# Kernel tuning notes

Measured on AMD Instinct MI355X. Metric: run time of the kernel, lower is better.

Reference implementation:

```python
import jax, jax.numpy as jnp
import numpy as np

B, K, H, W = 8, 32, 480, 480
N, D = 576, 1024
NUM_CLASSES, CLS_DIM, OUT = 150, 64, 256
IN_DIM = D + CLS_DIM + 5


def setup_inputs() -> dict:
    key = jax.random.key(0)
    ks = jax.random.split(key, 8)
    return {
        "feature_map": jax.random.normal(ks[0], (B, N, D), dtype=jnp.float32),
        "masks": jax.random.randint(ks[1], (B, K, H, W), 0, 2, dtype=jnp.int32),
        "class_ids": jax.random.randint(ks[2], (B, K), 0, NUM_CLASSES, dtype=jnp.int64),
        "embed_table": jax.random.normal(ks[3], (NUM_CLASSES, CLS_DIM), dtype=jnp.float32),
        "W1": jax.random.normal(ks[4], (IN_DIM, OUT), dtype=jnp.float32) * 0.02,
        "b1": jnp.zeros((OUT,), dtype=jnp.float32),
        "ln_g": jnp.ones((OUT,), dtype=jnp.float32),
        "ln_b": jnp.zeros((OUT,), dtype=jnp.float32),
        "W2": jax.random.normal(ks[5], (OUT, OUT), dtype=jnp.float32) * 0.02,
        "b2": jnp.zeros((OUT,), dtype=jnp.float32),
    }


def _geom_feats(m):
    # m: [B,K,H,W] float binary masks -> [B,K,5] (cx, cy, area_norm, bbox_w, bbox_h)
    dt = m.dtype
    area = m.sum((-2, -1))                      # [B,K]
    safe = jnp.maximum(area, 1.0)
    xs = jnp.arange(W, dtype=dt)
    ys = jnp.arange(H, dtype=dt)
    cx = jnp.einsum('bkhw,w->bk', m, xs) / safe / W
    cy = jnp.einsum('bkhw,h->bk', m, ys) / safe / H
    col = m.max(axis=2)                          # [B,K,W] column occupancy
    row = m.max(axis=3)                          # [B,K,H] row occupancy
    x_min = jnp.min(jnp.where(col > 0, xs, float(W)), axis=-1)
    x_max = jnp.max(jnp.where(col > 0, xs, -1.0), axis=-1)
    y_min = jnp.min(jnp.where(row > 0, ys, float(H)), axis=-1)
    y_max = jnp.max(jnp.where(row > 0, ys, -1.0), axis=-1)
    bbox_w = (x_max - x_min + 1.0) / W
    bbox_h = (y_max - y_min + 1.0) / H
    area_norm = area / (H * W)
    geom = jnp.stack([cx, cy, area_norm, bbox_w, bbox_h], axis=-1)  # [B,K,5]
    valid = (area >= 1.0)[..., None]
    return jnp.where(valid, geom, 0.0)


def reference(feature_map, masks, class_ids, embed_table, W1, b1, ln_g, ln_b, W2, b2):
    Hf = Wf = int(round(N ** 0.5))  # 24
    m = (masks > 0).astype(feature_map.dtype)           # [B,K,H,W]
    # nearest-neighbor downsample (PyTorch 'nearest': src = floor(dst*in/out))
    idx_h = (jnp.arange(Hf) * H) // Hf
    idx_w = (jnp.arange(Wf) * W) // Wf
    m_rs = m[:, :, idx_h][:, :, :, idx_w]               # [B,K,Hf,Wf]
    m_flat = m_rs.reshape(B, K, Hf * Wf)                # [B,K,N]
    msum = jnp.clip(m_flat.sum(-1, keepdims=True), 1e-6, None)
    pooled = jnp.einsum('bkn,bnd->bkd', m_flat, feature_map) / msum  # [B,K,D]
    geom = _geom_feats(m)                               # [B,K,5]
    cls_emb = embed_table[class_ids]                    # [B,K,CLS_DIM]
    x = jnp.concatenate([pooled, cls_emb, geom], axis=-1)  # [B,K,IN_DIM]
    h = jax.nn.gelu(x @ W1 + b1, approximate=False)
    mu = h.mean(-1, keepdims=True)
    var = jnp.mean((h - mu) ** 2, axis=-1, keepdims=True)
    hn = (h - mu) * jax.lax.rsqrt(var + 1e-5) * ln_g + ln_b
    return hn @ W2 + b2                                 # [B,K,OUT]
```

## Files before the change

### kernel.cpp

```cpp
#include <hip/hip_runtime.h>
#include <math.h>

#define Bb 8
#define Kk 32
#define Hh 480
#define Ww 480
#define Nn 576
#define Dd 1024
#define CLSD 64
#define OUTD 256
#define INDIM 1093
#define BK 256
#define PIX4 57600

__global__ __launch_bounds__(1024) void kF(const int* __restrict__ masks,
                                           const float* __restrict__ fm,
                                           const int* __restrict__ cids,
                                           const float* __restrict__ emb,
                                           const float* __restrict__ W1,
                                           const float* __restrict__ b1,
                                           const float* __restrict__ lg,
                                           const float* __restrict__ lb,
                                           const float* __restrict__ W2,
                                           const float* __restrict__ b2,
                                           float* __restrict__ out) {
  const int b    = blockIdx.x & 7;
  const int k    = blockIdx.x >> 3;
  const int bk   = b * Kk + k;
  const int t    = threadIdx.x;
  const int lane = t & 63;
  const int w    = t >> 6;

  __shared__ float  ds[576];
  __shared__ int    act[576];
  __shared__ float4 x4s[292];
  __shared__ float4 pp[4 * 256];
  __shared__ float  partial[16 * 256];
  __shared__ float  hrow[256];
  __shared__ float  red_s[16], red_q[16];
  __shared__ float  gmeta[8];
  __shared__ int s_area, s_sumx, s_sumy, s_cnt;
  __shared__ int s_minx, s_maxx, s_miny, s_maxy, nact;
  float* x = (float*)x4s;

  if (t == 0) {
    s_area = 0; s_sumx = 0; s_sumy = 0; s_cnt = 0;
    s_minx = Ww; s_maxx = -1; s_miny = Hh; s_maxy = -1;
    nact = 0;
  }
  __syncthreads();

  const int4* mp = (const int4*)(masks + (size_t)bk * (Hh * Ww));
  int area = 0, sumx = 0, sumy = 0, cntds = 0;
  int minx = Ww, maxx = -1, miny = Hh, maxy = -1;

  auto body = [&](int q, int4 v) {
    int h   = q / 120;
    int rem = q - h * 120;
    int w0  = rem * 4;
    int m0 = v.x > 0, m1 = v.y > 0, m2 = v.z > 0, m3 = v.w > 0;
    int c = m0 + m1 + m2 + m3;
    area += c;
    sumy += h * c;
    sumx += w0 * c + m1 + 2 * m2 + 3 * m3;
    if (c) {
      miny = min(miny, h);
      maxy = max(maxy, h);
      int lo = m0 ? w0 : (m1 ? w0 + 1 : (m2 ? w0 + 2 : w0 + 3));
      int hi = m3 ? w0 + 3 : (m2 ? w0 + 2 : (m1 ? w0 + 1 : w0));
      minx = min(minx, lo);
      maxx = max(maxx, hi);
    }
    int a20 = h / 20;
    int c5  = rem / 5;
    if (h == a20 * 20 && rem == c5 * 5) {
      ds[a20 * 24 + c5] = (float)m0;
      cntds += m0;
    }
  };

#pragma unroll 4
  for (int i = 0; i < 56; i++) {
    int q = t + (i << 10);
    body(q, mp[q]);
  }
  if (t < 256) {
    int q = 57344 + t;
    body(q, mp[q]);
  }

  for (int off = 32; off; off >>= 1) {
    area  += __shfl_down(area, off);
    sumx  += __shfl_down(sumx, off);
    sumy  += __shfl_down(sumy, off);
    cntds += __shfl_down(cntds, off);
    minx = min(minx, __shfl_down(minx, off));
    maxx = max(maxx, __shfl_down(maxx, off));
    miny = min(miny, __shfl_down(miny, off));
    maxy = max(maxy, __shfl_down(maxy, off));
  }
  if (lane == 0) {
    atomicAdd(&s_area, area);
    atomicAdd(&s_sumx, sumx);
    atomicAdd(&s_sumy, sumy);
    atomicAdd(&s_cnt, cntds);
    atomicMin(&s_minx, minx);
    atomicMax(&s_maxx, maxx);
    atomicMin(&s_miny, miny);
    atomicMax(&s_maxy, maxy);
  }
  __syncthreads();

  if (t == 0) {
    float areaf = (float)s_area;
    float safe  = fmaxf(areaf, 1.0f);
    float cx = ((float)s_sumx / safe) * (1.0f / Ww);
    float cy = ((float)s_sumy / safe) * (1.0f / Hh);
    float an = areaf * (1.0f / (Hh * Ww));
    float bw = (float)(s_maxx - s_minx + 1) * (1.0f / Ww);
    float bh = (float)(s_maxy - s_miny + 1) * (1.0f / Hh);
    if (s_area < 1) { cx = 0.f; cy = 0.f; an = 0.f; bw = 0.f; bh = 0.f; }
    gmeta[0] = cx; gmeta[1] = cy; gmeta[2] = an; gmeta[3] = bw; gmeta[4] = bh;
    gmeta[5] = 1.0f / fmaxf((float)s_cnt, 1e-6f);
  }
  if (t < 576 && ds[t] != 0.0f) act[atomicAdd(&nact, 1)] = t;
  if (t < 75) x[1093 + t] = 0.0f;
  __syncthreads();
  const int na = nact;

  {
    const int g   = t >> 8;
    const int col = t & 255;
    const int jb  = (na * g) >> 2;
    const int je  = (na * (g + 1)) >> 2;
    const float4* fmp = (const float4*)fm + (size_t)b * Nn * (Dd / 4);
    float ax = 0.f, ay = 0.f, az = 0.f, aw = 0.f;
    int j = jb;
    for (; j + 4 <= je; j += 4) {
      int n0 = act[j], n1 = act[j + 1], n2 = act[j + 2], n3 = act[j + 3];
      float4 f0 = fmp[n0 * (Dd / 4) + col];
      float4 f1 = fmp[n1 * (Dd / 4) + col];
      float4 f2 = fmp[n2 * (Dd / 4) + col];
      float4 f3 = fmp[n3 * (Dd / 4) + col];
      ax += f0.x + f1.x + f2.x + f3.x;
      ay += f0.y + f1.y + f2.y + f3.y;
      az += f0.z + f1.z + f2.z + f3.z;
      aw += f0.w + f1.w + f2.w + f3.w;
    }
    for (; j < je; j++) {
      float4 f = fmp[act[j] * (Dd / 4) + col];
      ax += f.x; ay += f.y; az += f.z; aw += f.w;
    }
    float4 p; p.x = ax; p.y = ay; p.z = az; p.w = aw;
    pp[g * 256 + col] = p;
  }
  __syncthreads();

  if (t < 256) {
    float inv = gmeta[5];
    float4 a0 = pp[t], a1 = pp[256 + t], a2 = pp[512 + t], a3 = pp[768 + t];
    float4 p;
    p.x = (a0.x + a1.x + a2.x + a3.x) * inv;
    p.y = (a0.y + a1.y + a2.y + a3.y) * inv;
    p.z = (a0.z + a1.z + a2.z + a3.z) * inv;
    p.w = (a0.w + a1.w + a2.w + a3.w) * inv;
    x4s[t] = p;
  } else if (t < 320) {
    x[Dd + (t - 256)] = emb[(size_t)cids[bk] * CLSD + (t - 256)];
  } else if (t < 325) {
    x[Dd + CLSD + (t - 320)] = gmeta[t - 320];
  }
  __syncthreads();

  {
    const int kbeg = w * 72;
    const int kend = min(INDIM, kbeg + 72);
    float4 acc = {0.f, 0.f, 0.f, 0.f};
    int kk = kbeg;
    for (; kk + 4 <= kend; kk += 4) {
      float4 xv = x4s[kk >> 2];
      const float* xs = (const float*)&xv;
#pragma unroll
      for (int u = 0; u < 4; u++) {
        float4 w4 = *(const float4*)(W1 + (size_t)(kk + u) * OUTD + 4 * lane);
        acc.x = fmaf(xs[u], w4.x, acc.x);
        acc.y = fmaf(xs[u], w4.y, acc.y);
        acc.z = fmaf(xs[u], w4.z, acc.z);
        acc.w = fmaf(xs[u], w4.w, acc.w);
      }
    }
    for (; kk < kend; kk++) {
      float xv = x[kk];
      float4 w4 = *(const float4*)(W1 + (size_t)kk * OUTD + 4 * lane);
      acc.x = fmaf(xv, w4.x, acc.x);
      acc.y = fmaf(xv, w4.y, acc.y);
      acc.z = fmaf(xv, w4.z, acc.z);
      acc.w = fmaf(xv, w4.w, acc.w);
    }
    *(float4*)(partial + w * 256 + 4 * lane) = acc;
  }
  __syncthreads();

  float hv = 0.f;
  if (t < 256) {
    hv = b1[t];
#pragma unroll
    for (int ww = 0; ww < 16; ww++) hv += partial[ww * 256 + t];
    hv = 0.5f * hv * (1.0f + erff(hv * 0.7071067811865475f));
  }
  {
    float s = hv, q = hv * hv;
    for (int off = 32; off; off >>= 1) {
      s += __shfl_down(s, off);
      q += __shfl_down(q, off);
    }
    if (lane == 0) { red_s[w] = s; red_q[w] = q; }
  }
  __syncthreads();
  if (t < 256) {
    float s = 0.f, q = 0.f;
#pragma unroll
    for (int ww = 0; ww < 16; ww++) { s += red_s[ww]; q += red_q[ww]; }
    float mu  = s * (1.0f / OUTD);
    float var = q * (1.0f / OUTD) - mu * mu;
    float ist = 1.0f / sqrtf(var + 1e-5f);
    hrow[t] = (hv - mu) * ist * lg[t] + lb[t];
  }
  __syncthreads();

  {
    float4 acc = {0.f, 0.f, 0.f, 0.f};
#pragma unroll
    for (int i = 0; i < 4; i++) {
      float4 h4 = ((const float4*)hrow)[w * 4 + i];
      const float* hs = (const float*)&h4;
#pragma unroll
      for (int u = 0; u < 4; u++) {
        int kk = w * 16 + i * 4 + u;
        float4 w4 = *(const float4*)(W2 + (size_t)kk * OUTD + 4 * lane);
        acc.x = fmaf(hs[u], w4.x, acc.x);
        acc.y = fmaf(hs[u], w4.y, acc.y);
        acc.z = fmaf(hs[u], w4.z, acc.z);
        acc.w = fmaf(hs[u], w4.w, acc.w);
      }
    }
    *(float4*)(partial + w * 256 + 4 * lane) = acc;
  }
  __syncthreads();

  if (t < 256) {
    float c = b2[t];
#pragma unroll
    for (int ww = 0; ww < 16; ww++) c += partial[ww * 256 + t];
    out[(size_t)bk * OUTD + t] = c;
  }
}

extern "C" void kernel_launch(void* const* d_in, const int* in_sizes, int n_in,
                              void* d_out, int out_size, void* d_ws, size_t ws_size,
                              hipStream_t stream) {
  const float* fm    = (const float*)d_in[0];
  const int*   masks = (const int*)d_in[1];
  const int*   cids  = (const int*)d_in[2];
  const float* emb   = (const float*)d_in[3];
  const float* W1    = (const float*)d_in[4];
  const float* b1    = (const float*)d_in[5];
  const float* lg    = (const float*)d_in[6];
  const float* lb    = (const float*)d_in[7];
  const float* W2    = (const float*)d_in[8];
  const float* b2    = (const float*)d_in[9];
  float* out = (float*)d_out;

  hipLaunchKernelGGL(kF, dim3(BK), dim3(1024), 0, stream, masks, fm, cids, emb,
                     W1, b1, lg, lb, W2, b2, out);
}
```

Baseline: 374.5 us.

## Warp-specialize mask stats and feature pooling/W1 GEMV to overlap

The mask sampling for the downsampled active list now happens first, with 576 direct gathers of the sampled pixels. After that the block is split: 12 warps stream the full mask for the geometry statistics, while 4 warps pool the feature rows and compute the pooled part of the W1 GEMV at the same time. The class-embedding and geometry terms of W1 are folded into the per-output epilogue, which removes several block-wide syncs and shared buffers. The risk is load imbalance: only 4 warps now carry the feature gather plus the 1024x256 W1 product, so that path may become the critical path.

```diff
diff --git a/kernel.cpp b/kernel.cpp
--- a/kernel.cpp
+++ b/kernel.cpp
@@ -31,83 +31,115 @@
   const int lane = t & 63;
   const int w    = t >> 6;
 
-  __shared__ float  ds[576];
   __shared__ int    act[576];
-  __shared__ float4 x4s[292];
-  __shared__ float4 pp[4 * 256];
+  __shared__ float4 x4s[256];
   __shared__ float  partial[16 * 256];
   __shared__ float  hrow[256];
-  __shared__ float  red_s[16], red_q[16];
+  __shared__ float  red_s[4], red_q[4];
   __shared__ float  gmeta[8];
-  __shared__ int s_area, s_sumx, s_sumy, s_cnt;
+  __shared__ int s_area, s_sumx, s_sumy;
   __shared__ int s_minx, s_maxx, s_miny, s_maxy, nact;
-  float* x = (float*)x4s;
 
   if (t == 0) {
-    s_area = 0; s_sumx = 0; s_sumy = 0; s_cnt = 0;
+    s_area = 0; s_sumx = 0; s_sumy = 0;
     s_minx = Ww; s_maxx = -1; s_miny = Hh; s_maxy = -1;
     nact = 0;
   }
   __syncthreads();
 
-  const int4* mp = (const int4*)(masks + (size_t)bk * (Hh * Ww));
-  int area = 0, sumx = 0, sumy = 0, cntds = 0;
-  int minx = Ww, maxx = -1, miny = Hh, maxy = -1;
-
-  auto body = [&](int q, int4 v) {
-    int h   = q / 120;
-    int rem = q - h * 120;
-    int w0  = rem * 4;
-    int m0 = v.x > 0, m1 = v.y > 0, m2 = v.z > 0, m3 = v.w > 0;
-    int c = m0 + m1 + m2 + m3;
-    area += c;
-    sumy += h * c;
-    sumx += w0 * c + m1 + 2 * m2 + 3 * m3;
-    if (c) {
-      miny = min(miny, h);
-      maxy = max(maxy, h);
-      int lo = m0 ? w0 : (m1 ? w0 + 1 : (m2 ? w0 + 2 : w0 + 3));
-      int hi = m3 ? w0 + 3 : (m2 ? w0 + 2 : (m1 ? w0 + 1 : w0));
-      minx = min(minx, lo);
-      maxx = max(maxx, hi);
-    }
-    int a20 = h / 20;
-    int c5  = rem / 5;
-    if (h == a20 * 20 && rem == c5 * 5) {
-      ds[a20 * 24 + c5] = (float)m0;
-      cntds += m0;
-    }
-  };
-
-#pragma unroll 4
-  for (int i = 0; i < 56; i++) {
-    int q = t + (i << 10);
-    body(q, mp[q]);
-  }
-  if (t < 256) {
-    int q = 57344 + t;
-    body(q, mp[q]);
-  }
-
-  for (int off = 32; off; off >>= 1) {
-    area  += __shfl_down(area, off);
-    sumx  += __shfl_down(sumx, off);
-    sumy  += __shfl_down(sumy, off);
-    cntds += __shfl_down(cntds, off);
-    minx = min(minx, __shfl_down(minx, off));
-    maxx = max(maxx, __shfl_down(maxx, off));
-    miny = min(miny, __shfl_down(miny, off));
-    maxy = max(maxy, __shfl_down(maxy, off));
-  }
-  if (lane == 0) {
-    atomicAdd(&s_area, area);
-    atomicAdd(&s_sumx, sumx);
-    atomicAdd(&s_sumy, sumy);
-    atomicAdd(&s_cnt, cntds);
-    atomicMin(&s_minx, minx);
-    atomicMax(&s_maxx, maxx);
-    atomicMin(&s_miny, miny);
-    atomicMax(&s_maxy, maxy);
+  const int* mbase = masks + (size_t)bk * (Hh * Ww);
+  if (t < 576) {
+    int a = t / 24, c = t - a * 24;
+    if (mbase[a * 20 * Ww + c * 20] > 0) act[atomicAdd(&nact, 1)] = t;
+  }
+  __syncthreads();
+  const int na = nact;
+
+  if (w < 12) {
+    int area = 0, sumx = 0, sumy = 0;
+    int minx = Ww, maxx = -1, miny = Hh, maxy = -1;
+    const int4* mp = (const int4*)mbase;
+#pragma unroll 5
+    for (int i = 0; i < 75; i++) {
+      int q = t + i * 768;
+      int4 v = mp[q];
+      int h   = q / 120;
+      int rem = q - h * 120;
+      int w0  = rem * 4;
+      int m0 = v.x > 0, m1 = v.y > 0, m2 = v.z > 0, m3 = v.w > 0;
+      int c = m0 + m1 + m2 + m3;
+      area += c;
+      sumy += h * c;
+      sumx += w0 * c + m1 + 2 * m2 + 3 * m3;
+      if (c) {
+        miny = min(miny, h);
+        maxy = max(maxy, h);
+        int lo = m0 ? w0 : (m1 ? w0 + 1 : (m2 ? w0 + 2 : w0 + 3));
+        int hi = m3 ? w0 + 3 : (m2 ? w0 + 2 : (m1 ? w0 + 1 : w0));
+        minx = min(minx, lo);
+        maxx = max(maxx, hi);
+      }
+    }
+    for (int off = 32; off; off >>= 1) {
+      area += __shfl_down(area, off);
+      sumx += __shfl_down(sumx, off);
+      sumy += __shfl_down(sumy, off);
+      minx = min(minx, __shfl_down(minx, off));
+      maxx = max(maxx, __shfl_down(maxx, off));
+      miny = min(miny, __shfl_down(miny, off));
+      maxy = max(maxy, __shfl_down(maxy, off));
+    }
+    if (lane == 0) {
+      atomicAdd(&s_area, area);
+      atomicAdd(&s_sumx, sumx);
+      atomicAdd(&s_sumy, sumy);
+      atomicMin(&s_minx, minx);
+      atomicMax(&s_maxx, maxx);
+      atomicMin(&s_miny, miny);
+      atomicMax(&s_maxy, maxy);
+    }
+  } else {
+    const int cw   = w - 12;
+    const int base = cw * 64 + lane;
+    const float4* fmp = (const float4*)fm + (size_t)b * Nn * (Dd / 4);
+    float ax = 0.f, ay = 0.f, az = 0.f, aw = 0.f;
+    int j = 0;
+    for (; j + 4 <= na; j += 4) {
+      int n0 = act[j], n1 = act[j + 1], n2 = act[j + 2], n3 = act[j + 3];
+      float4 f0 = fmp[n0 * (Dd / 4) + base];
+      float4 f1 = fmp[n1 * (Dd / 4) + base];
+      float4 f2 = fmp[n2 * (Dd / 4) + base];
+      float4 f3 = fmp[n3 * (Dd / 4) + base];
+      ax += f0.x + f1.x + f2.x + f3.x;
+      ay += f0.y + f1.y + f2.y + f3.y;
+      az += f0.z + f1.z + f2.z + f3.z;
+      aw += f0.w + f1.w + f2.w + f3.w;
+    }
+    for (; j < na; j++) {
+      float4 f = fmp[act[j] * (Dd / 4) + base];
+      ax += f.x; ay += f.y; az += f.z; aw += f.w;
+    }
+    float inv = 1.0f / fmaxf((float)na, 1e-6f);
+    float4 xp;
+    xp.x = ax * inv; xp.y = ay * inv; xp.z = az * inv; xp.w = aw * inv;
+    x4s[base] = xp;
+
+    float4 acc = {0.f, 0.f, 0.f, 0.f};
+    const float* W1b = W1 + (size_t)(cw * 256) * OUTD + 4 * lane;
+#pragma unroll 2
+    for (int g = 0; g < 64; g++) {
+      float4 xv = x4s[cw * 64 + g];
+      const float* xs = (const float*)&xv;
+#pragma unroll
+      for (int u = 0; u < 4; u++) {
+        float4 w4 = *(const float4*)(W1b + (size_t)(4 * g + u) * OUTD);
+        acc.x = fmaf(xs[u], w4.x, acc.x);
+        acc.y = fmaf(xs[u], w4.y, acc.y);
+        acc.z = fmaf(xs[u], w4.z, acc.z);
+        acc.w = fmaf(xs[u], w4.w, acc.w);
+      }
+    }
+    *(float4*)(partial + cw * 256 + 4 * lane) = acc;
   }
   __syncthreads();
 
@@ -121,91 +153,19 @@
     float bh = (float)(s_maxy - s_miny + 1) * (1.0f / Hh);
     if (s_area < 1) { cx = 0.f; cy = 0.f; an = 0.f; bw = 0.f; bh = 0.f; }
     gmeta[0] = cx; gmeta[1] = cy; gmeta[2] = an; gmeta[3] = bw; gmeta[4] = bh;
-    gmeta[5] = 1.0f / fmaxf((float)s_cnt, 1e-6f);
-  }
-  if (t < 576 && ds[t] != 0.0f) act[atomicAdd(&nact, 1)] = t;
-  if (t < 75) x[1093 + t] = 0.0f;
-  __syncthreads();
-  const int na = nact;
-
-  {
-    const int g   = t >> 8;
-    const int col = t & 255;
-    const int jb  = (na * g) >> 2;
-    const int je  = (na * (g + 1)) >> 2;
-    const float4* fmp = (const float4*)fm + (size_t)b * Nn * (Dd / 4);
-    float ax = 0.f, ay = 0.f, az = 0.f, aw = 0.f;
-    int j = jb;
-    for (; j + 4 <= je; j += 4) {
-      int n0 = act[j], n1 = act[j + 1], n2 = act[j + 2], n3 = act[j + 3];
-      float4 f0 = fmp[n0 * (Dd / 4) + col];
-      float4 f1 = fmp[n1 * (Dd / 4) + col];
-      float4 f2 = fmp[n2 * (Dd / 4) + col];
-      float4 f3 = fmp[n3 * (Dd / 4) + col];
-      ax += f0.x + f1.x + f2.x + f3.x;
-      ay += f0.y + f1.y + f2.y + f3.y;
-      az += f0.z + f1.z + f2.z + f3.z;
-      aw += f0.w + f1.w + f2.w + f3.w;
-    }
-    for (; j < je; j++) {
-      float4 f = fmp[act[j] * (Dd / 4) + col];
-      ax += f.x; ay += f.y; az += f.z; aw += f.w;
-    }
-    float4 p; p.x = ax; p.y = ay; p.z = az; p.w = aw;
-    pp[g * 256 + col] = p;
-  }
-  __syncthreads();
-
-  if (t < 256) {
-    float inv = gmeta[5];
-    float4 a0 = pp[t], a1 = pp[256 + t], a2 = pp[512 + t], a3 = pp[768 + t];
-    float4 p;
-    p.x = (a0.x + a1.x + a2.x + a3.x) * inv;
-    p.y = (a0.y + a1.y + a2.y + a3.y) * inv;
-    p.z = (a0.z + a1.z + a2.z + a3.z) * inv;
-    p.w = (a0.w + a1.w + a2.w + a3.w) * inv;
-    x4s[t] = p;
-  } else if (t < 320) {
-    x[Dd + (t - 256)] = emb[(size_t)cids[bk] * CLSD + (t - 256)];
-  } else if (t < 325) {
-    x[Dd + CLSD + (t - 320)] = gmeta[t - 320];
-  }
-  __syncthreads();
-
-  {
-    const int kbeg = w * 72;
-    const int kend = min(INDIM, kbeg + 72);
-    float4 acc = {0.f, 0.f, 0.f, 0.f};
-    int kk = kbeg;
-    for (; kk + 4 <= kend; kk += 4) {
-      float4 xv = x4s[kk >> 2];
-      const float* xs = (const float*)&xv;
-#pragma unroll
-      for (int u = 0; u < 4; u++) {
-        float4 w4 = *(const float4*)(W1 + (size_t)(kk + u) * OUTD + 4 * lane);
-        acc.x = fmaf(xs[u], w4.x, acc.x);
-        acc.y = fmaf(xs[u], w4.y, acc.y);
-        acc.z = fmaf(xs[u], w4.z, acc.z);
-        acc.w = fmaf(xs[u], w4.w, acc.w);
-      }
-    }
-    for (; kk < kend; kk++) {
-      float xv = x[kk];
-      float4 w4 = *(const float4*)(W1 + (size_t)kk * OUTD + 4 * lane);
-      acc.x = fmaf(xv, w4.x, acc.x);
-      acc.y = fmaf(xv, w4.y, acc.y);
-      acc.z = fmaf(xv, w4.z, acc.z);
-      acc.w = fmaf(xv, w4.w, acc.w);
-    }
-    *(float4*)(partial + w * 256 + 4 * lane) = acc;
   }
   __syncthreads();
 
   float hv = 0.f;
   if (t < 256) {
-    hv = b1[t];
-#pragma unroll
-    for (int ww = 0; ww < 16; ww++) hv += partial[ww * 256 + t];
+    hv = b1[t] + partial[t] + partial[256 + t] + partial[512 + t] + partial[768 + t];
+    const float* et = emb + (size_t)cids[bk] * CLSD;
+#pragma unroll 8
+    for (int i = 0; i < CLSD; i++)
+      hv = fmaf(et[i], W1[(size_t)(Dd + i) * OUTD + t], hv);
+#pragma unroll
+    for (int jj = 0; jj < 5; jj++)
+      hv = fmaf(gmeta[jj], W1[(size_t)(Dd + CLSD + jj) * OUTD + t], hv);
     hv = 0.5f * hv * (1.0f + erff(hv * 0.7071067811865475f));
   }
   {
@@ -214,13 +174,12 @@
       s += __shfl_down(s, off);
       q += __shfl_down(q, off);
     }
-    if (lane == 0) { red_s[w] = s; red_q[w] = q; }
+    if (lane == 0 && w < 4) { red_s[w] = s; red_q[w] = q; }
   }
   __syncthreads();
   if (t < 256) {
-    float s = 0.f, q = 0.f;
-#pragma unroll
-    for (int ww = 0; ww < 16; ww++) { s += red_s[ww]; q += red_q[ww]; }
+    float s = red_s[0] + red_s[1] + red_s[2] + red_s[3];
+    float q = red_q[0] + red_q[1] + red_q[2] + red_q[3];
     float mu  = s * (1.0f / OUTD);
     float var = q * (1.0f / OUTD) - mu * mu;
     float ist = 1.0f / sqrtf(var + 1e-5f);
```

Measured after the change: 372.9 us. Within noise of the previous version (-0.4%).
